# Kernel optimization log

Measured on AMD Instinct MI355X. Metric: run time of the kernel, lower is better.

The kernel has to match this reference:

```python
import jax, jax.numpy as jnp
import numpy as np

B, H, W, C = 2, 64, 64, 192
NUM_HEADS = 6
K = 7  # kernel_size, dilation = 1


def setup_inputs() -> dict:
    key = jax.random.key(0)
    ks = jax.random.split(key, 5)
    return {
        "x": jax.random.normal(ks[0], (B, H, W, C), dtype=jnp.float32),
        "w_qkv": jax.random.normal(ks[1], (3 * C, C), dtype=jnp.float32) * 0.02,
        "rpb": jax.random.normal(ks[2], (NUM_HEADS, 2 * K - 1, 2 * K - 1), dtype=jnp.float32) * 0.02,
        "temperature": jnp.ones((NUM_HEADS,), dtype=jnp.float32),
        "w_proj": jax.random.normal(ks[3], (C, C), dtype=jnp.float32) * 0.02,
    }


def reference(x, w_qkv, rpb, temperature, w_proj):
    b, h, w, c = x.shape
    hd = c // NUM_HEADS
    scale = hd ** (-0.5)

    # 1x1 conv qkv projection (pointwise linear over channels)
    qkv = jnp.einsum("bhwc,dc->bhwd", x, w_qkv)
    qkv = qkv.reshape(b, h, w, 3, NUM_HEADS, hd).transpose(3, 0, 4, 1, 2, 5)
    q, k, v = qkv[0], qkv[1], qkv[2]  # (B, nH, H, W, hd)
    q = q * scale

    # NATTEN neighborhood: window centered at each pixel, clamped to stay in-bounds
    si = jnp.clip(jnp.arange(h) - K // 2, 0, h - K)
    rows = si[:, None] + jnp.arange(K)          # (H, K) neighbor row indices
    sj = jnp.clip(jnp.arange(w) - K // 2, 0, w - K)
    cols = sj[:, None] + jnp.arange(K)          # (W, K) neighbor col indices

    # gather key/value neighborhoods: (B, nH, H, K, W, K, hd)
    k_nb = k[:, :, rows][:, :, :, :, cols]
    v_nb = v[:, :, rows][:, :, :, :, cols]

    # QK: (B, nH, H, W, Kh, Kw)
    attn = jnp.einsum("bnijd,bnikjld->bnijkl", q, k_nb)

    # relative position bias: index = neighbor - query + (K-1)
    ri = rows - jnp.arange(h)[:, None] + (K - 1)  # (H, K)
    rj = cols - jnp.arange(w)[:, None] + (K - 1)  # (W, K)
    bias = rpb[:, ri][:, :, :, rj]                # (nH, H, K, W, K)
    bias = bias.transpose(0, 1, 3, 2, 4)          # (nH, H, W, K, K)
    attn = attn + bias[None]

    attn = attn.reshape(b, NUM_HEADS, h, w, K * K)
    attn = attn * temperature[None, :, None, None, None]
    attn = jax.nn.softmax(attn, axis=-1)

    v_nb = v_nb.transpose(0, 1, 2, 4, 3, 5, 6).reshape(b, NUM_HEADS, h, w, K * K, hd)
    out = jnp.einsum("bnijp,bnijpd->bnijd", attn, v_nb)
    out = out.transpose(0, 2, 3, 1, 4).reshape(b, h, w, c)

    # 1x1 conv output projection
    return jnp.einsum("bhwc,dc->bhwd", out, w_proj)
```

## Files before the change

### kernel.cpp

```cpp
#include <hip/hip_runtime.h>
#include <hip/hip_bf16.h>
#include <math.h>

#define BB 2
#define HH 64
#define WW 64
#define CC 192
#define NH 6
#define HD 32
#define KS 7
#define NPIX 8192
#define SCALE 0.17677669529663687f

typedef __attribute__((ext_vector_type(8))) _Float16 f16x8;
typedef __attribute__((ext_vector_type(4))) _Float16 f16x4;
typedef __attribute__((ext_vector_type(2))) _Float16 h2;
typedef __attribute__((ext_vector_type(4))) float    f32x4;

#if defined(__has_builtin) && __has_builtin(__builtin_amdgcn_fdot2)
#define FDOT2(a, b, c) __builtin_amdgcn_fdot2((a), (b), (c), false)
#else
#define FDOT2(a, b, c) fmaf((float)(a)[0], (float)(b)[0], fmaf((float)(a)[1], (float)(b)[1], (c)))
#endif

#define XN   1572864
#define OFF_XH  0
#define OFF_WQ  1572864
#define OFF_WP  1683456
#define OFF_QKV 1720320
#define OFF_ATT 6438912

__global__ __launch_bounds__(256) void cvt_f16(const float* __restrict__ x,
                                               const float* __restrict__ wq,
                                               const float* __restrict__ wp,
                                               _Float16* __restrict__ dst) {
    const size_t off = ((size_t)blockIdx.x * 256 + threadIdx.x) * 4;
    float4 v;
    if (off < XN)                 v = *(const float4*)(x  + off);
    else if (off < OFF_WP)        v = *(const float4*)(wq + (off - OFF_WQ));
    else                          v = *(const float4*)(wp + (off - OFF_WP));
    f16x4 h = {(_Float16)v.x, (_Float16)v.y, (_Float16)v.z, (_Float16)v.w};
    *(f16x4*)(dst + off) = h;
}

__global__ __launch_bounds__(256) void gemm_h(const _Float16* __restrict__ A,
                                              const _Float16* __restrict__ B,
                                              _Float16* __restrict__ Ch,
                                              float* __restrict__ Cf,
                                              int N) {
    const int t    = threadIdx.x;
    const int row0 = blockIdx.x * 64;
    const int col0 = blockIdx.y * 64;
    const int wave = t >> 6;
    const int wr   = wave >> 1;
    const int wc   = wave & 1;
    const int ln   = t & 15;
    const int quad = (t & 63) >> 4;

    f32x4 acc[2][2] = {};

#pragma unroll
    for (int ks = 0; ks < 6; ++ks) {
        const int k0 = ks * 32 + quad * 8;
        f16x8 af[2], bf[2];
        af[0] = *(const f16x8*)(A + (size_t)(row0 + wr * 32 + ln) * 192 + k0);
        af[1] = *(const f16x8*)(A + (size_t)(row0 + wr * 32 + 16 + ln) * 192 + k0);
        bf[0] = *(const f16x8*)(B + (size_t)(col0 + wc * 32 + ln) * 192 + k0);
        bf[1] = *(const f16x8*)(B + (size_t)(col0 + wc * 32 + 16 + ln) * 192 + k0);
#pragma unroll
        for (int mi = 0; mi < 2; ++mi)
#pragma unroll
            for (int ni = 0; ni < 2; ++ni)
                acc[mi][ni] = __builtin_amdgcn_mfma_f32_16x16x32_f16(
                    af[mi], bf[ni], acc[mi][ni], 0, 0, 0);
    }

#pragma unroll
    for (int mi = 0; mi < 2; ++mi)
#pragma unroll
        for (int ni = 0; ni < 2; ++ni) {
            const int col = col0 + wc * 32 + ni * 16 + ln;
#pragma unroll
            for (int r = 0; r < 4; ++r) {
                const int row = row0 + wr * 32 + mi * 16 + quad * 4 + r;
                if (Ch) Ch[(size_t)row * N + col] = (_Float16)acc[mi][ni][r];
                else    Cf[(size_t)row * N + col] = acc[mi][ni][r];
            }
        }
}

#define PL   264
#define ROWU (8 * PL)

__global__ __launch_bounds__(256) void natten_v4(const _Float16* __restrict__ qkv,
                                                 const float* __restrict__ rpb,
                                                 const float* __restrict__ temperature,
                                                 _Float16* __restrict__ outh) {
    const int tid  = threadIdx.x;
    const int w    = tid >> 6;
    const int j    = tid & 63;
    const int i    = blockIdx.x & 63;
    const int head = (blockIdx.x >> 6) % NH;
    const int b    = blockIdx.x / 384;

    __shared__ unsigned region[4][2][ROWU];
    __shared__ float srpb[169];

    const float temp = temperature[head];
    const float st   = SCALE * temp;
    if (tid < 169) srpb[tid] = rpb[head * 169 + tid] * temp;

    const int pix = b * 4096 + i * 64 + j;
    const _Float16* qp = qkv + (size_t)pix * 576 + head * HD;
    h2 qh[16];
    {
        uint4 q0 = *(const uint4*)(qp +  0);
        uint4 q1 = *(const uint4*)(qp +  8);
        uint4 q2 = *(const uint4*)(qp + 16);
        uint4 q3 = *(const uint4*)(qp + 24);
        *(uint4*)&qh[0]  = q0; *(uint4*)&qh[4]  = q1;
        *(uint4*)&qh[8]  = q2; *(uint4*)&qh[12] = q3;
    }

    __syncthreads();

    const int si = min(max(i - 3, 0), HH - KS);
    const int sj = min(max(j - 3, 0), WW - KS);

    float l = 0.f;
    float acc[HD];
#pragma unroll
    for (int d = 0; d < HD; ++d) acc[d] = 0.f;

    const int nrows = (w < 3) ? 2 : 1;
    for (int t = 0; t < nrows; ++t) {
        const int ni = si + 2 * w + t;

        const _Float16* rb0 = qkv + ((size_t)(b * 4096 + ni * 64)) * 576 + 192 + head * HD;
        unsigned* reg = &region[w][t][0];
#pragma unroll
        for (int it = 0; it < 8; ++it) {
            const int idx = j + (it << 6);
            const int px = idx >> 3, c = idx & 7;
            uint4 d = *(const uint4*)(rb0 + (size_t)px * 576 + (c >> 2) * 192 + (c & 3) * 8);
            *(uint4*)&reg[c * PL + px * 4] = d;
        }

        const float* rbias = srpb + (ni - i + 6) * 13;
#pragma unroll
        for (int kj = 0; kj < 7; ++kj) {
            const int nj = sj + kj;
            const unsigned* pp = reg + nj * 4;

            h2 kh[16];
            *(uint4*)&kh[0]  = *(const uint4*)(pp + 0 * PL);
            *(uint4*)&kh[4]  = *(const uint4*)(pp + 1 * PL);
            *(uint4*)&kh[8]  = *(const uint4*)(pp + 2 * PL);
            *(uint4*)&kh[12] = *(const uint4*)(pp + 3 * PL);

            float d0 = 0.f, d1 = 0.f, d2 = 0.f, d3 = 0.f;
#pragma unroll
            for (int c = 0; c < 4; ++c) {
                d0 = FDOT2(qh[c * 4 + 0], kh[c * 4 + 0], d0);
                d1 = FDOT2(qh[c * 4 + 1], kh[c * 4 + 1], d1);
                d2 = FDOT2(qh[c * 4 + 2], kh[c * 4 + 2], d2);
                d3 = FDOT2(qh[c * 4 + 3], kh[c * 4 + 3], d3);
            }
            const float dot = (d0 + d1) + (d2 + d3);
            const float p = __expf(fmaf(dot, st, rbias[nj - j + 6]));
            l += p;

            h2 vh[16];
            *(uint4*)&vh[0]  = *(const uint4*)(pp + 4 * PL);
            *(uint4*)&vh[4]  = *(const uint4*)(pp + 5 * PL);
            *(uint4*)&vh[8]  = *(const uint4*)(pp + 6 * PL);
            *(uint4*)&vh[12] = *(const uint4*)(pp + 7 * PL);
#pragma unroll
            for (int c = 0; c < 16; ++c) {
                acc[2 * c + 0] = fmaf((float)vh[c][0], p, acc[2 * c + 0]);
                acc[2 * c + 1] = fmaf((float)vh[c][1], p, acc[2 * c + 1]);
            }
        }
    }

    if (w > 0) {
        float* mp = (float*)&region[w][0][0] + j * 33;
#pragma unroll
        for (int d = 0; d < 32; ++d) mp[d] = acc[d];
        mp[32] = l;
    }
    __syncthreads();
    if (w == 0) {
#pragma unroll
        for (int ww = 1; ww < 4; ++ww) {
            const float* mp = (const float*)&region[ww][0][0] + j * 33;
#pragma unroll
            for (int d = 0; d < 32; ++d) acc[d] += mp[d];
            l += mp[32];
        }
        const float inv = 1.f / l;
        _Float16* op = outh + (size_t)pix * CC + head * HD;
        unsigned o[16];
#pragma unroll
        for (int c = 0; c < 16; ++c) {
            h2 pk;
            pk[0] = (_Float16)(acc[2 * c + 0] * inv);
            pk[1] = (_Float16)(acc[2 * c + 1] * inv);
            o[c] = *(unsigned*)&pk;
        }
        *(uint4*)(op +  0) = *(uint4*)&o[0];
        *(uint4*)(op +  8) = *(uint4*)&o[4];
        *(uint4*)(op + 16) = *(uint4*)&o[8];
        *(uint4*)(op + 24) = *(uint4*)&o[12];
    }
}

extern "C" void kernel_launch(void* const* d_in, const int* in_sizes, int n_in,
                              void* d_out, int out_size, void* d_ws, size_t ws_size,
                              hipStream_t stream) {
    const float* x           = (const float*)d_in[0];
    const float* w_qkv       = (const float*)d_in[1];
    const float* rpb         = (const float*)d_in[2];
    const float* temperature = (const float*)d_in[3];
    const float* w_proj      = (const float*)d_in[4];
    float* out = (float*)d_out;

    _Float16* hws    = (_Float16*)d_ws;
    _Float16* x_h    = hws + OFF_XH;
    _Float16* wq_h   = hws + OFF_WQ;
    _Float16* wp_h   = hws + OFF_WP;
    _Float16* qkv_h  = hws + OFF_QKV;
    _Float16* attn_h = hws + OFF_ATT;

    cvt_f16<<<dim3(1680), 256, 0, stream>>>(x, w_qkv, w_proj, hws);

    gemm_h<<<dim3(128, 9), 256, 0, stream>>>(x_h, wq_h, qkv_h, nullptr, 3 * CC);

    natten_v4<<<dim3(768), 256, 0, stream>>>(qkv_h, rpb, temperature, attn_h);

    gemm_h<<<dim3(128, 3), 256, 0, stream>>>(attn_h, wp_h, nullptr, out, CC);
}
```

Baseline: 114.4 us.

## Fuse pipeline into one cooperative persistent kernel with in-register f16 conversion

```diff
diff --git a/kernel.cpp b/kernel.cpp
--- a/kernel.cpp
+++ b/kernel.cpp
@@ -1,4 +1,5 @@
 #include <hip/hip_runtime.h>
+#include <hip/hip_cooperative_groups.h>
 #include <hip/hip_bf16.h>
 #include <math.h>
 
@@ -13,7 +14,6 @@
 #define SCALE 0.17677669529663687f
 
 typedef __attribute__((ext_vector_type(8))) _Float16 f16x8;
-typedef __attribute__((ext_vector_type(4))) _Float16 f16x4;
 typedef __attribute__((ext_vector_type(2))) _Float16 h2;
 typedef __attribute__((ext_vector_type(4))) float    f32x4;
 
@@ -23,105 +23,74 @@
 #define FDOT2(a, b, c) fmaf((float)(a)[0], (float)(b)[0], fmaf((float)(a)[1], (float)(b)[1], (c)))
 #endif
 
-#define XN   1572864
-#define OFF_XH  0
-#define OFF_WQ  1572864
-#define OFF_WP  1683456
-#define OFF_QKV 1720320
-#define OFF_ATT 6438912
-
-__global__ __launch_bounds__(256) void cvt_f16(const float* __restrict__ x,
-                                               const float* __restrict__ wq,
-                                               const float* __restrict__ wp,
-                                               _Float16* __restrict__ dst) {
-    const size_t off = ((size_t)blockIdx.x * 256 + threadIdx.x) * 4;
-    float4 v;
-    if (off < XN)                 v = *(const float4*)(x  + off);
-    else if (off < OFF_WP)        v = *(const float4*)(wq + (off - OFF_WQ));
-    else                          v = *(const float4*)(wp + (off - OFF_WP));
-    f16x4 h = {(_Float16)v.x, (_Float16)v.y, (_Float16)v.z, (_Float16)v.w};
-    *(f16x4*)(dst + off) = h;
-}
-
-__global__ __launch_bounds__(256) void gemm_h(const _Float16* __restrict__ A,
-                                              const _Float16* __restrict__ B,
-                                              _Float16* __restrict__ Ch,
-                                              float* __restrict__ Cf,
-                                              int N) {
-    const int t    = threadIdx.x;
-    const int row0 = blockIdx.x * 64;
-    const int col0 = blockIdx.y * 64;
-    const int wave = t >> 6;
-    const int wr   = wave >> 1;
-    const int wc   = wave & 1;
-    const int ln   = t & 15;
-    const int quad = (t & 63) >> 4;
-
-    f32x4 acc[2][2] = {};
-
-#pragma unroll
-    for (int ks = 0; ks < 6; ++ks) {
-        const int k0 = ks * 32 + quad * 8;
-        f16x8 af[2], bf[2];
-        af[0] = *(const f16x8*)(A + (size_t)(row0 + wr * 32 + ln) * 192 + k0);
-        af[1] = *(const f16x8*)(A + (size_t)(row0 + wr * 32 + 16 + ln) * 192 + k0);
-        bf[0] = *(const f16x8*)(B + (size_t)(col0 + wc * 32 + ln) * 192 + k0);
-        bf[1] = *(const f16x8*)(B + (size_t)(col0 + wc * 32 + 16 + ln) * 192 + k0);
+__device__ __forceinline__ f16x8 cvt8(const float* p) {
+    float4 u0 = *(const float4*)p;
+    float4 u1 = *(const float4*)(p + 4);
+    f16x8 h = {(_Float16)u0.x, (_Float16)u0.y, (_Float16)u0.z, (_Float16)u0.w,
+               (_Float16)u1.x, (_Float16)u1.y, (_Float16)u1.z, (_Float16)u1.w};
+    return h;
+}
+
+__device__ __forceinline__ void phase_gemm1(int bid, int t,
+                                            const float* __restrict__ x,
+                                            const float* __restrict__ wq,
+                                            _Float16* __restrict__ qkv) {
+    const int tm   = bid & 127;
+    const int g    = bid >> 7;
+    const int wave = t >> 6, wr = wave >> 1, wc = wave & 1;
+    const int ln   = t & 15, quad = (t & 63) >> 4;
+
+    f16x8 af[2][6];
+#pragma unroll
+    for (int mi = 0; mi < 2; ++mi) {
+        const float* ar = x + (size_t)(tm * 64 + wr * 32 + mi * 16 + ln) * 192;
+#pragma unroll
+        for (int ks = 0; ks < 6; ++ks)
+            af[mi][ks] = cvt8(ar + ks * 32 + quad * 8);
+    }
+
+#pragma unroll
+    for (int r = 0; r < 3; ++r) {
+        const int tn = g + 6 * r;
+        const int n  = tn * 32 + wc * 16 + ln;
+        const float* br = wq + (size_t)n * 192;
+        f32x4 acc[2] = {};
+#pragma unroll
+        for (int ks = 0; ks < 6; ++ks) {
+            f16x8 bf = cvt8(br + ks * 32 + quad * 8);
+            acc[0] = __builtin_amdgcn_mfma_f32_16x16x32_f16(af[0][ks], bf, acc[0], 0, 0, 0);
+            acc[1] = __builtin_amdgcn_mfma_f32_16x16x32_f16(af[1][ks], bf, acc[1], 0, 0, 0);
+        }
 #pragma unroll
         for (int mi = 0; mi < 2; ++mi)
 #pragma unroll
-            for (int ni = 0; ni < 2; ++ni)
-                acc[mi][ni] = __builtin_amdgcn_mfma_f32_16x16x32_f16(
-                    af[mi], bf[ni], acc[mi][ni], 0, 0, 0);
-    }
-
-#pragma unroll
-    for (int mi = 0; mi < 2; ++mi)
-#pragma unroll
-        for (int ni = 0; ni < 2; ++ni) {
-            const int col = col0 + wc * 32 + ni * 16 + ln;
-#pragma unroll
-            for (int r = 0; r < 4; ++r) {
-                const int row = row0 + wr * 32 + mi * 16 + quad * 4 + r;
-                if (Ch) Ch[(size_t)row * N + col] = (_Float16)acc[mi][ni][r];
-                else    Cf[(size_t)row * N + col] = acc[mi][ni][r];
-            }
-        }
-}
-
-#define PL   264
-#define ROWU (8 * PL)
-
-__global__ __launch_bounds__(256) void natten_v4(const _Float16* __restrict__ qkv,
-                                                 const float* __restrict__ rpb,
-                                                 const float* __restrict__ temperature,
-                                                 _Float16* __restrict__ outh) {
-    const int tid  = threadIdx.x;
-    const int w    = tid >> 6;
-    const int j    = tid & 63;
-    const int i    = blockIdx.x & 63;
-    const int head = (blockIdx.x >> 6) % NH;
-    const int b    = blockIdx.x / 384;
-
-    __shared__ unsigned region[4][2][ROWU];
-    __shared__ float srpb[169];
-
-    const float temp = temperature[head];
-    const float st   = SCALE * temp;
-    if (tid < 169) srpb[tid] = rpb[head * 169 + tid] * temp;
+            for (int rg = 0; rg < 4; ++rg)
+                qkv[(size_t)(tm * 64 + wr * 32 + mi * 16 + quad * 4 + rg) * 576 + n] =
+                    (_Float16)acc[mi][rg];
+    }
+}
+
+__device__ __forceinline__ void phase_natten(int bid, int t,
+                                             const _Float16* __restrict__ qkv,
+                                             const float* __restrict__ rpb,
+                                             const float* __restrict__ temperature,
+                                             _Float16* __restrict__ outh,
+                                             unsigned (*region)[2112],
+                                             float* srpb) {
+    const int w = t >> 6, j = t & 63;
+    const int i = bid & 63, head = (bid >> 6) % NH, b = bid / 384;
+
+    const float tp = temperature[head];
+    const float st = SCALE * tp;
+    if (t < 169) srpb[t] = rpb[head * 169 + t] * tp;
 
     const int pix = b * 4096 + i * 64 + j;
     const _Float16* qp = qkv + (size_t)pix * 576 + head * HD;
     h2 qh[16];
-    {
-        uint4 q0 = *(const uint4*)(qp +  0);
-        uint4 q1 = *(const uint4*)(qp +  8);
-        uint4 q2 = *(const uint4*)(qp + 16);
-        uint4 q3 = *(const uint4*)(qp + 24);
-        *(uint4*)&qh[0]  = q0; *(uint4*)&qh[4]  = q1;
-        *(uint4*)&qh[8]  = q2; *(uint4*)&qh[12] = q3;
-    }
-
+    *(uint4*)&qh[0]  = *(const uint4*)(qp);
+    *(uint4*)&qh[4]  = *(const uint4*)(qp + 8);
+    *(uint4*)&qh[8]  = *(const uint4*)(qp + 16);
+    *(uint4*)&qh[12] = *(const uint4*)(qp + 24);
     __syncthreads();
 
     const int si = min(max(i - 3, 0), HH - KS);
@@ -132,31 +101,31 @@
 #pragma unroll
     for (int d = 0; d < HD; ++d) acc[d] = 0.f;
 
+    unsigned* reg = region[w];
     const int nrows = (w < 3) ? 2 : 1;
-    for (int t = 0; t < nrows; ++t) {
-        const int ni = si + 2 * w + t;
-
-        const _Float16* rb0 = qkv + ((size_t)(b * 4096 + ni * 64)) * 576 + 192 + head * HD;
-        unsigned* reg = &region[w][t][0];
+    for (int r = 0; r < nrows; ++r) {
+        const int ni = si + 2 * w + r;
+
+        const _Float16* rb0 = qkv + (size_t)(b * 4096 + ni * 64) * 576 + 192 + head * HD;
 #pragma unroll
         for (int it = 0; it < 8; ++it) {
             const int idx = j + (it << 6);
             const int px = idx >> 3, c = idx & 7;
             uint4 d = *(const uint4*)(rb0 + (size_t)px * 576 + (c >> 2) * 192 + (c & 3) * 8);
-            *(uint4*)&reg[c * PL + px * 4] = d;
+            *(uint4*)&reg[px * 33 + c * 4] = d;
         }
 
         const float* rbias = srpb + (ni - i + 6) * 13;
 #pragma unroll
         for (int kj = 0; kj < 7; ++kj) {
             const int nj = sj + kj;
-            const unsigned* pp = reg + nj * 4;
+            const unsigned* pp = reg + nj * 33;
 
             h2 kh[16];
-            *(uint4*)&kh[0]  = *(const uint4*)(pp + 0 * PL);
-            *(uint4*)&kh[4]  = *(const uint4*)(pp + 1 * PL);
-            *(uint4*)&kh[8]  = *(const uint4*)(pp + 2 * PL);
-            *(uint4*)&kh[12] = *(const uint4*)(pp + 3 * PL);
+            *(uint4*)&kh[0]  = *(const uint4*)(pp + 0);
+            *(uint4*)&kh[4]  = *(const uint4*)(pp + 4);
+            *(uint4*)&kh[8]  = *(const uint4*)(pp + 8);
+            *(uint4*)&kh[12] = *(const uint4*)(pp + 12);
 
             float d0 = 0.f, d1 = 0.f, d2 = 0.f, d3 = 0.f;
 #pragma unroll
@@ -171,10 +140,10 @@
             l += p;
 
             h2 vh[16];
-            *(uint4*)&vh[0]  = *(const uint4*)(pp + 4 * PL);
-            *(uint4*)&vh[4]  = *(const uint4*)(pp + 5 * PL);
-            *(uint4*)&vh[8]  = *(const uint4*)(pp + 6 * PL);
-            *(uint4*)&vh[12] = *(const uint4*)(pp + 7 * PL);
+            *(uint4*)&vh[0]  = *(const uint4*)(pp + 16);
+            *(uint4*)&vh[4]  = *(const uint4*)(pp + 20);
+            *(uint4*)&vh[8]  = *(const uint4*)(pp + 24);
+            *(uint4*)&vh[12] = *(const uint4*)(pp + 28);
 #pragma unroll
             for (int c = 0; c < 16; ++c) {
                 acc[2 * c + 0] = fmaf((float)vh[c][0], p, acc[2 * c + 0]);
@@ -184,18 +153,18 @@
     }
 
     if (w > 0) {
-        float* mp = (float*)&region[w][0][0] + j * 33;
-#pragma unroll
-        for (int d = 0; d < 32; ++d) mp[d] = acc[d];
+        float* mp = (float*)region[w] + j * 33;
+#pragma unroll
+        for (int d = 0; d < HD; ++d) mp[d] = acc[d];
         mp[32] = l;
     }
     __syncthreads();
     if (w == 0) {
 #pragma unroll
         for (int ww = 1; ww < 4; ++ww) {
-            const float* mp = (const float*)&region[ww][0][0] + j * 33;
-#pragma unroll
-            for (int d = 0; d < 32; ++d) acc[d] += mp[d];
+            const float* mp = (const float*)region[ww] + j * 33;
+#pragma unroll
+            for (int d = 0; d < HD; ++d) acc[d] += mp[d];
             l += mp[32];
         }
         const float inv = 1.f / l;
@@ -213,6 +182,69 @@
         *(uint4*)(op + 16) = *(uint4*)&o[8];
         *(uint4*)(op + 24) = *(uint4*)&o[12];
     }
+    __syncthreads();
+}
+
+__device__ __forceinline__ void phase_gemm2(int bid, int t,
+                                            const _Float16* __restrict__ attn,
+                                            const float* __restrict__ wp,
+                                            float* __restrict__ out) {
+    const int tm = bid / 6, tn = bid % 6;
+    const int wave = t >> 6, wr = wave >> 1, wc = wave & 1;
+    const int ln = t & 15, quad = (t & 63) >> 4;
+
+    const int n = tn * 32 + wc * 16 + ln;
+    const _Float16* ar0 = attn + (size_t)(tm * 64 + wr * 32 + ln) * 192;
+    const _Float16* ar1 = attn + (size_t)(tm * 64 + wr * 32 + 16 + ln) * 192;
+    const float* br = wp + (size_t)n * 192;
+
+    f32x4 acc[2] = {};
+#pragma unroll
+    for (int ks = 0; ks < 6; ++ks) {
+        const int k0 = ks * 32 + quad * 8;
+        f16x8 a0 = *(const f16x8*)(ar0 + k0);
+        f16x8 a1 = *(const f16x8*)(ar1 + k0);
+        f16x8 bf = cvt8(br + k0);
+        acc[0] = __builtin_amdgcn_mfma_f32_16x16x32_f16(a0, bf, acc[0], 0, 0, 0);
+        acc[1] = __builtin_amdgcn_mfma_f32_16x16x32_f16(a1, bf, acc[1], 0, 0, 0);
+    }
+#pragma unroll
+    for (int mi = 0; mi < 2; ++mi)
+#pragma unroll
+        for (int rg = 0; rg < 4; ++rg)
+            out[(size_t)(tm * 64 + wr * 32 + mi * 16 + quad * 4 + rg) * 192 + n] = acc[mi][rg];
+}
+
+__global__ __launch_bounds__(256, 3) void mega(const float* __restrict__ x,
+                                               const float* __restrict__ wq,
+                                               const float* __restrict__ rpb,
+                                               const float* __restrict__ temp,
+                                               const float* __restrict__ wp,
+                                               _Float16* __restrict__ qkv,
+                                               _Float16* __restrict__ attn,
+                                               float* __restrict__ out) {
+    __shared__ unsigned region[4][2112];
+    __shared__ float srpb[169];
+    const int bid = blockIdx.x, t = threadIdx.x;
+
+    phase_gemm1(bid, t, x, wq, qkv);
+    cooperative_groups::this_grid().sync();
+    phase_natten(bid, t, qkv, rpb, temp, attn, region, srpb);
+    cooperative_groups::this_grid().sync();
+    phase_gemm2(bid, t, attn, wp, out);
+}
+
+__global__ __launch_bounds__(256, 3) void p1k(const float* x, const float* wq, _Float16* qkv) {
+    phase_gemm1(blockIdx.x, threadIdx.x, x, wq, qkv);
+}
+__global__ __launch_bounds__(256, 3) void p2k(const _Float16* qkv, const float* rpb,
+                                              const float* temp, _Float16* attn) {
+    __shared__ unsigned region[4][2112];
+    __shared__ float srpb[169];
+    phase_natten(blockIdx.x, threadIdx.x, qkv, rpb, temp, attn, region, srpb);
+}
+__global__ __launch_bounds__(256, 3) void p3k(const _Float16* attn, const float* wp, float* out) {
+    phase_gemm2(blockIdx.x, threadIdx.x, attn, wp, out);
 }
 
 extern "C" void kernel_launch(void* const* d_in, const int* in_sizes, int n_in,
@@ -225,18 +257,16 @@
     const float* w_proj      = (const float*)d_in[4];
     float* out = (float*)d_out;
 
-    _Float16* hws    = (_Float16*)d_ws;
-    _Float16* x_h    = hws + OFF_XH;
-    _Float16* wq_h   = hws + OFF_WQ;
-    _Float16* wp_h   = hws + OFF_WP;
-    _Float16* qkv_h  = hws + OFF_QKV;
-    _Float16* attn_h = hws + OFF_ATT;
-
-    cvt_f16<<<dim3(1680), 256, 0, stream>>>(x, w_qkv, w_proj, hws);
-
-    gemm_h<<<dim3(128, 9), 256, 0, stream>>>(x_h, wq_h, qkv_h, nullptr, 3 * CC);
-
-    natten_v4<<<dim3(768), 256, 0, stream>>>(qkv_h, rpb, temperature, attn_h);
-
-    gemm_h<<<dim3(128, 3), 256, 0, stream>>>(attn_h, wp_h, nullptr, out, CC);
-}
+    _Float16* qkv_h  = (_Float16*)d_ws;
+    _Float16* attn_h = qkv_h + (size_t)NPIX * 3 * CC;
+
+    void* args[8] = {(void*)&x, (void*)&w_qkv, (void*)&rpb, (void*)&temperature,
+                     (void*)&w_proj, (void*)&qkv_h, (void*)&attn_h, (void*)&out};
+    hipError_t e = hipLaunchCooperativeKernel((const void*)mega, dim3(768), dim3(256),
+                                              (void**)args, 0, stream);
+    if (e != hipSuccess) {
+        p1k<<<dim3(768), 256, 0, stream>>>(x, w_qkv, qkv_h);
+        p2k<<<dim3(768), 256, 0, stream>>>(qkv_h, rpb, temperature, attn_h);
+        p3k<<<dim3(768), 256, 0, stream>>>(attn_h, w_proj, out);
+    }
+}
```

Measured after the change: 340.1 us. 197% more time.
